# Kernel tuning notes

Hardware: AMD Instinct MI355X
Metric: run time of the kernel (lower is better)

Reference implementation:

```python
import jax, jax.numpy as jnp
import numpy as np

VOCAB = 32000
EMBED = 256
HID = 512
SOS_ID = 1
EOS_ID = 2
PAD_ID = 0


def setup_inputs() -> dict:
    key = jax.random.key(0)
    ks = jax.random.split(key, 8)
    B, L = 64, 49
    scale = 0.02
    return {
        "features": jax.random.normal(ks[0], (B, L, HID), jnp.float32),
        "emb": jax.random.normal(ks[1], (VOCAB, EMBED), jnp.float32) * scale,
        "W_ih": jax.random.normal(ks[2], (3 * HID, EMBED), jnp.float32) * scale,
        "W_hh": jax.random.normal(ks[3], (3 * HID, HID), jnp.float32) * scale,
        "b_ih": jax.random.normal(ks[4], (3 * HID,), jnp.float32) * scale,
        "b_hh": jax.random.normal(ks[5], (3 * HID,), jnp.float32) * scale,
        "W_out": jax.random.normal(ks[6], (VOCAB, HID), jnp.float32) * scale,
        "b_out": jax.random.normal(ks[7], (VOCAB,), jnp.float32) * scale,
        "max_len": 20,
    }


def _gru_cell(x, h, W_ih, W_hh, b_ih, b_hh):
    # torch.nn.GRUCell semantics (gates ordered r, z, n)
    gi = x @ W_ih.T + b_ih  # [B, 3H]
    gh = h @ W_hh.T + b_hh  # [B, 3H]
    i_r, i_z, i_n = jnp.split(gi, 3, axis=-1)
    h_r, h_z, h_n = jnp.split(gh, 3, axis=-1)
    r = jax.nn.sigmoid(i_r + h_r)
    z = jax.nn.sigmoid(i_z + h_z)
    n = jnp.tanh(i_n + r * h_n)
    return (1.0 - z) * n + z * h


def reference(features, emb, W_ih, W_hh, b_ih, b_hh, W_out, b_out, max_len):
    B = features.shape[0]
    h0 = features.mean(axis=1)  # [B, HID]
    x0 = emb[jnp.full((B,), SOS_ID, dtype=jnp.int32)]  # [B, EMBED]
    done0 = jnp.zeros((B,), dtype=bool)

    def step(carry, _):
        h, x, done = carry
        h = _gru_cell(x, h, W_ih, W_hh, b_ih, b_hh)
        logits = h @ W_out.T + b_out  # [B, VOCAB]
        pred = jnp.argmax(logits, axis=-1)  # [B]
        is_eos = pred == EOS_ID
        # original appends word only if sequence not complete and token != <EOS>
        tok = jnp.where(done | is_eos, PAD_ID, pred)
        done = done | is_eos
        x = emb[pred]  # greedy feedback
        return (h, x, done), (logits, tok)

    _, (logits, toks) = jax.lax.scan(step, (h0, x0, done0), None, length=max_len)
    # [T, B, V] -> [B, T, V]; [T, B] -> [B, T]
    return toks.T, jnp.transpose(logits, (1, 0, 2))
```

## Files before the change

### kernel.cpp

```cpp
#include <hip/hip_runtime.h>
#include <stdint.h>

#define VOCABN 32000
#define EMBEDN 256
#define HIDN   512
#define BN     64
#define SOSID  1
#define EOSID  2
#define NSUB   8

typedef __attribute__((ext_vector_type(8))) short short8;
typedef __attribute__((ext_vector_type(4))) float f32x4;

__device__ __forceinline__ unsigned ordf(float f) {
  unsigned u = __float_as_uint(f);
  return (u & 0x80000000u) ? ~u : (u | 0x80000000u);
}
__device__ __forceinline__ int decode_pred(unsigned long long pk) {
  return (int)(0xFFFFFFFFu - (unsigned)(pk & 0xFFFFFFFFull));
}
__device__ __forceinline__ unsigned short f2bf(float x) {
  unsigned u = __float_as_uint(x);
  unsigned r = (u + 0x7FFFu + ((u >> 16) & 1u)) >> 16;
  return (unsigned short)r;
}
__device__ __forceinline__ float bf2f(unsigned short h) {
  return __uint_as_float(((unsigned)h) << 16);
}
__device__ __forceinline__ f32x4 mfma3(short8 ah, short8 al, short8 bh, short8 bl,
                                       f32x4 acc) {
  acc = __builtin_amdgcn_mfma_f32_16x16x32_bf16(ah, bh, acc, 0, 0, 0);
  acc = __builtin_amdgcn_mfma_f32_16x16x32_bf16(ah, bl, acc, 0, 0, 0);
  acc = __builtin_amdgcn_mfma_f32_16x16x32_bf16(al, bh, acc, 0, 0, 0);
  return acc;
}

__global__ void k_init(const float* __restrict__ feat, float* __restrict__ h0,
                       int L, int* __restrict__ done, char* __restrict__ Hsp0) {
  int b = blockIdx.x, tid = threadIdx.x;
  float inv = 1.0f / (float)L;
  for (int j = tid; j < HIDN; j += 256) {
    const float* p = feat + (size_t)b * L * HIDN + j;
    float s = 0.f;
    for (int l = 0; l < L; ++l) s += p[(size_t)l * HIDN];
    float hv = s * inv;
    h0[b * HIDN + j] = hv;
    unsigned short hi = f2bf(hv);
    unsigned short lo = f2bf(hv - bf2f(hi));
    int bt = b >> 4, col = b & 15, kt = j >> 5, kr = j & 31;
    int ln = ((kr >> 3) << 4) | col, e = kr & 7;
    size_t off = (size_t)(bt * 16 + kt) * 2048 + ln * 16 + e * 2;
    *(unsigned short*)(Hsp0 + off) = hi;
    *(unsigned short*)(Hsp0 + off + 1024) = lo;
  }
  if (b == 0 && tid < 2 * BN) done[tid] = 0;
}

__global__ __launch_bounds__(256) void k_splitW(const float* __restrict__ W,
                                                char* __restrict__ Wsp,
                                                int ktshift, int K) {
  int tid = threadIdx.x, lane = tid & 63, tl = tid >> 6;
  int tile = blockIdx.x * 4 + tl;
  int vt = tile >> ktshift, kt = tile & ((1 << ktshift) - 1);
  int v = vt * 16 + (lane & 15);
  int k0 = kt * 32 + ((lane >> 4) << 3);
  const float* src = W + (size_t)v * K + k0;
  float xv[8];
  *(float4*)&xv[0] = *(const float4*)src;
  *(float4*)&xv[4] = *(const float4*)(src + 4);
  unsigned short h[8], l[8];
  #pragma unroll
  for (int i = 0; i < 8; ++i) {
    h[i] = f2bf(xv[i]);
    l[i] = f2bf(xv[i] - bf2f(h[i]));
  }
  uint4 H, Lw;
  H.x = (unsigned)h[0] | ((unsigned)h[1] << 16);
  H.y = (unsigned)h[2] | ((unsigned)h[3] << 16);
  H.z = (unsigned)h[4] | ((unsigned)h[5] << 16);
  H.w = (unsigned)h[6] | ((unsigned)h[7] << 16);
  Lw.x = (unsigned)l[0] | ((unsigned)l[1] << 16);
  Lw.y = (unsigned)l[2] | ((unsigned)l[3] << 16);
  Lw.z = (unsigned)l[4] | ((unsigned)l[5] << 16);
  Lw.w = (unsigned)l[6] | ((unsigned)l[7] << 16);
  char* dst = Wsp + (size_t)tile * 2048 + lane * 16;
  *(uint4*)dst = H;
  *(uint4*)(dst + 1024) = Lw;
}

__global__ __launch_bounds__(256) void k_gh(
    const float* __restrict__ emb, const char* __restrict__ Wihsp,
    const char* __restrict__ Whhsp, const float* __restrict__ b_ih,
    const float* __restrict__ b_hh, const float* __restrict__ h_rd,
    float* __restrict__ h_wr, const char* __restrict__ Hsp_rd,
    char* __restrict__ Hsp_wr,
    const unsigned long long* __restrict__ s_rd,
    unsigned long long* __restrict__ s_wr,
    const int* __restrict__ done_rd, int* __restrict__ done_wr,
    float* __restrict__ out_toks, int t, int T) {
  __shared__ int preds[16];
  __shared__ float red[3][4][256];
  int tid = threadIdx.x, lane = tid & 63, wid = tid >> 6;
  int jt = blockIdx.x >> 2, bt = blockIdx.x & 3;

  if (tid < 16) {
    int pr = SOSID;
    if (t) {
      unsigned long long mx = 0ull;
      #pragma unroll
      for (int s = 0; s < NSUB; ++s) {
        unsigned long long v = s_rd[s * BN + bt * 16 + tid];
        mx = (v > mx) ? v : mx;
      }
      pr = decode_pred(mx);
    }
    preds[tid] = pr;
  }
  if (blockIdx.x == 0) {
    s_wr[tid] = 0ull;
    s_wr[256 + tid] = 0ull;
    if (t >= 1 && tid < BN) {
      unsigned long long mx = 0ull;
      #pragma unroll
      for (int s = 0; s < NSUB; ++s) {
        unsigned long long v = s_rd[s * BN + tid];
        mx = (v > mx) ? v : mx;
      }
      int pred = decode_pred(mx);
      int iseos = (pred == EOSID) ? 1 : 0;
      int dold = done_rd[tid];
      out_toks[(size_t)tid * T + (t - 1)] = (float)((dold | iseos) ? 0 : pred);
      done_wr[tid] = dold | iseos;
    }
  }
  __syncthreads();

  int col = lane & 15, rg = lane >> 4;
  int xrow = preds[col];
  f32x4 acc_r = {0.f, 0.f, 0.f, 0.f}, acc_z = {0.f, 0.f, 0.f, 0.f};
  f32x4 acc_gin = {0.f, 0.f, 0.f, 0.f}, acc_ghn = {0.f, 0.f, 0.f, 0.f};

  #pragma unroll
  for (int u = 0; u < 6; ++u) {
    int g = wid * 6 + u;
    if (g < 8) {
      float xv[8];
      const float* src = emb + (size_t)xrow * EMBEDN + g * 32 + rg * 8;
      *(float4*)&xv[0] = *(const float4*)src;
      *(float4*)&xv[4] = *(const float4*)(src + 4);
      unsigned short hi[8], lo[8];
      #pragma unroll
      for (int i = 0; i < 8; ++i) {
        hi[i] = f2bf(xv[i]);
        lo[i] = f2bf(xv[i] - bf2f(hi[i]));
      }
      short8 xh, xl;
      #pragma unroll
      for (int i = 0; i < 8; ++i) { xh[i] = (short)hi[i]; xl[i] = (short)lo[i]; }
      const char* pr_ = Wihsp + (size_t)((jt) * 8 + g) * 2048 + lane * 16;
      const char* pz_ = Wihsp + (size_t)((32 + jt) * 8 + g) * 2048 + lane * 16;
      const char* pn_ = Wihsp + (size_t)((64 + jt) * 8 + g) * 2048 + lane * 16;
      acc_r = mfma3(*(const short8*)pr_, *(const short8*)(pr_ + 1024), xh, xl, acc_r);
      acc_z = mfma3(*(const short8*)pz_, *(const short8*)(pz_ + 1024), xh, xl, acc_z);
      acc_gin = mfma3(*(const short8*)pn_, *(const short8*)(pn_ + 1024), xh, xl, acc_gin);
    } else {
      int kt = g - 8;
      const char* bq = Hsp_rd + (size_t)(bt * 16 + kt) * 2048 + lane * 16;
      short8 hh = *(const short8*)bq;
      short8 hl = *(const short8*)(bq + 1024);
      const char* pr_ = Whhsp + (size_t)((jt) * 16 + kt) * 2048 + lane * 16;
      const char* pz_ = Whhsp + (size_t)((32 + jt) * 16 + kt) * 2048 + lane * 16;
      const char* pn_ = Whhsp + (size_t)((64 + jt) * 16 + kt) * 2048 + lane * 16;
      acc_r = mfma3(*(const short8*)pr_, *(const short8*)(pr_ + 1024), hh, hl, acc_r);
      acc_z = mfma3(*(const short8*)pz_, *(const short8*)(pz_ + 1024), hh, hl, acc_z);
      acc_ghn = mfma3(*(const short8*)pn_, *(const short8*)(pn_ + 1024), hh, hl, acc_ghn);
    }
  }

  if (wid) {
    *(f32x4*)&red[wid - 1][0][lane * 4] = acc_r;
    *(f32x4*)&red[wid - 1][1][lane * 4] = acc_z;
    *(f32x4*)&red[wid - 1][2][lane * 4] = acc_gin;
    *(f32x4*)&red[wid - 1][3][lane * 4] = acc_ghn;
  }
  __syncthreads();
  if (wid == 0) {
    #pragma unroll
    for (int w = 0; w < 3; ++w) {
      acc_r += *(f32x4*)&red[w][0][lane * 4];
      acc_z += *(f32x4*)&red[w][1][lane * 4];
      acc_gin += *(f32x4*)&red[w][2][lane * 4];
      acc_ghn += *(f32x4*)&red[w][3][lane * 4];
    }
    int j0 = jt * 16, j = j0 + rg * 4;
    int b = bt * 16 + col;
    float4 bir = *(const float4*)(b_ih + j);
    float4 bhr = *(const float4*)(b_hh + j);
    float4 biz = *(const float4*)(b_ih + 512 + j);
    float4 bhz = *(const float4*)(b_hh + 512 + j);
    float4 bin = *(const float4*)(b_ih + 1024 + j);
    float4 bhn = *(const float4*)(b_hh + 1024 + j);
    float bra[4] = {bir.x + bhr.x, bir.y + bhr.y, bir.z + bhr.z, bir.w + bhr.w};
    float bza[4] = {biz.x + bhz.x, biz.y + bhz.y, biz.z + bhz.z, biz.w + bhz.w};
    float bia[4] = {bin.x, bin.y, bin.z, bin.w};
    float bha[4] = {bhn.x, bhn.y, bhn.z, bhn.w};
    float4 hold = *(const float4*)(h_rd + (size_t)b * HIDN + j);
    float ho[4] = {hold.x, hold.y, hold.z, hold.w};
    float hn[4];
    unsigned short hi[4], lo[4];
    #pragma unroll
    for (int reg = 0; reg < 4; ++reg) {
      float r = 1.f / (1.f + expf(-(acc_r[reg] + bra[reg])));
      float z = 1.f / (1.f + expf(-(acc_z[reg] + bza[reg])));
      float n = tanhf(acc_gin[reg] + bia[reg] + r * (acc_ghn[reg] + bha[reg]));
      hn[reg] = (1.f - z) * n + z * ho[reg];
      hi[reg] = f2bf(hn[reg]);
      lo[reg] = f2bf(hn[reg] - bf2f(hi[reg]));
    }
    float4 hout = {hn[0], hn[1], hn[2], hn[3]};
    *(float4*)(h_wr + (size_t)b * HIDN + j) = hout;
    int kt2 = j >> 5, kr2 = j & 31;
    int ln2 = ((kr2 >> 3) << 4) | col, e2 = kr2 & 7;
    char* dst = Hsp_wr + ((size_t)((b >> 4) * 16 + kt2) * 2048 + ln2 * 16 + e2 * 2);
    uint2 Hp, Lp;
    Hp.x = (unsigned)hi[0] | ((unsigned)hi[1] << 16);
    Hp.y = (unsigned)hi[2] | ((unsigned)hi[3] << 16);
    Lp.x = (unsigned)lo[0] | ((unsigned)lo[1] << 16);
    Lp.y = (unsigned)lo[2] | ((unsigned)lo[3] << 16);
    *(uint2*)dst = Hp;
    *(uint2*)(dst + 1024) = Lp;
  }
}

__global__ __launch_bounds__(256) void k_logits6(
    const char* __restrict__ Wsp, const char* __restrict__ Hsp,
    const float* __restrict__ bout, float* __restrict__ out_logits,
    unsigned long long* __restrict__ slots, int t, int T) {
  __shared__ __align__(16) f32x4 red[4][4][2][64];
  int tid = threadIdx.x, lane = tid & 63, wid = tid >> 6;
  int v0 = blockIdx.x * 32, vt = v0 >> 4;
  int sub = blockIdx.x & (NSUB - 1);

  f32x4 acc[4][2];
  #pragma unroll
  for (int nb = 0; nb < 4; ++nb)
    #pragma unroll
    for (int mv = 0; mv < 2; ++mv)
      acc[nb][mv] = (f32x4){0.f, 0.f, 0.f, 0.f};

  #pragma unroll 2
  for (int kk = 0; kk < 4; ++kk) {
    int kt = wid * 4 + kk;
    short8 ah[4], al[4], wh[2], wl[2];
    #pragma unroll
    for (int nb = 0; nb < 4; ++nb) {
      const char* q = Hsp + (size_t)(nb * 16 + kt) * 2048 + lane * 16;
      ah[nb] = *(const short8*)q;
      al[nb] = *(const short8*)(q + 1024);
    }
    #pragma unroll
    for (int mv = 0; mv < 2; ++mv) {
      const char* p = Wsp + (size_t)((vt + mv) * 16 + kt) * 2048 + lane * 16;
      wh[mv] = *(const short8*)p;
      wl[mv] = *(const short8*)(p + 1024);
    }
    #pragma unroll
    for (int nb = 0; nb < 4; ++nb)
      #pragma unroll
      for (int mv = 0; mv < 2; ++mv)
        acc[nb][mv] = mfma3(ah[nb], al[nb], wh[mv], wl[mv], acc[nb][mv]);
  }

  #pragma unroll
  for (int nb = 0; nb < 4; ++nb)
    #pragma unroll
    for (int mv = 0; mv < 2; ++mv)
      red[wid][nb][mv][lane] = acc[nb][mv];
  __syncthreads();

  int nb = wid;
  f32x4 sum[2];
  #pragma unroll
  for (int mv = 0; mv < 2; ++mv)
    sum[mv] = red[0][nb][mv][lane] + red[1][nb][mv][lane] +
              red[2][nb][mv][lane] + red[3][nb][mv][lane];

  int col = lane & 15, rg = lane >> 4;
  float bvv[2] = {bout[v0 + col], bout[v0 + 16 + col]};
  unsigned long long key[4] = {0ull, 0ull, 0ull, 0ull};

  #pragma unroll
  for (int mv = 0; mv < 2; ++mv) {
    int v = v0 + mv * 16 + col;
    #pragma unroll
    for (int reg = 0; reg < 4; ++reg) {
      float val = sum[mv][reg] + bvv[mv];
      int b = nb * 16 + rg * 4 + reg;
      __builtin_nontemporal_store(
          val, out_logits + ((size_t)b * T + t) * VOCABN + v);
      unsigned long long pk = ((unsigned long long)ordf(val) << 32) |
                              (unsigned long long)(0xFFFFFFFFu - (unsigned)v);
      key[reg] = (pk > key[reg]) ? pk : key[reg];
    }
  }
  #pragma unroll
  for (int m = 1; m < 16; m <<= 1) {
    #pragma unroll
    for (int reg = 0; reg < 4; ++reg) {
      unsigned long long o = __shfl_xor(key[reg], m, 64);
      key[reg] = (o > key[reg]) ? o : key[reg];
    }
  }
  if (col == 0) {
    #pragma unroll
    for (int reg = 0; reg < 4; ++reg) {
      int b = nb * 16 + rg * 4 + reg;
      atomicMax(slots + sub * BN + b, key[reg]);
    }
  }
}

__global__ void k_final(const unsigned long long* __restrict__ slots,
                        const int* __restrict__ done_rd,
                        float* __restrict__ out_toks, int T) {
  int b = threadIdx.x;
  if (b < BN) {
    unsigned long long mx = 0ull;
    #pragma unroll
    for (int s = 0; s < NSUB; ++s) {
      unsigned long long v = slots[s * BN + b];
      mx = (v > mx) ? v : mx;
    }
    int pred = decode_pred(mx);
    int iseos = (pred == EOSID) ? 1 : 0;
    int tok = (done_rd[b] || iseos) ? 0 : pred;
    out_toks[(size_t)b * T + (T - 1)] = (float)tok;
  }
}

extern "C" void kernel_launch(void* const* d_in, const int* in_sizes, int n_in,
                              void* d_out, int out_size, void* d_ws, size_t ws_size,
                              hipStream_t stream) {
  const float* feat = (const float*)d_in[0];
  const float* emb  = (const float*)d_in[1];
  const float* W_ih = (const float*)d_in[2];
  const float* W_hh = (const float*)d_in[3];
  const float* b_ih = (const float*)d_in[4];
  const float* b_hh = (const float*)d_in[5];
  const float* Wout = (const float*)d_in[6];
  const float* bout = (const float*)d_in[7];

  int L = in_sizes[0] / (BN * HIDN);
  int T = out_size / (BN * (VOCABN + 1));
  if (T <= 0) T = 20;

  float* out_toks   = (float*)d_out;
  float* out_logits = (float*)d_out + (size_t)BN * T;

  char* w = (char*)d_ws;
  float* hbuf = (float*)w;  w += (size_t)2 * BN * HIDN * sizeof(float);
  int*   done = (int*)w;    w += (size_t)2 * BN * sizeof(int);
  w = (char*)(((uintptr_t)w + 511) & ~(uintptr_t)511);
  unsigned long long* slots2 = (unsigned long long*)w;
  w += (size_t)2 * NSUB * BN * sizeof(unsigned long long);
  w = (char*)(((uintptr_t)w + 511) & ~(uintptr_t)511);
  char* Hsp   = w;          w += (size_t)2 * 4 * 16 * 2048;
  char* Wihsp = w;          w += (size_t)96 * 8 * 2048;
  char* Whhsp = w;          w += (size_t)96 * 16 * 2048;
  char* Wsp   = w;          w += (size_t)2000 * 16 * 2048;

  k_init<<<BN, 256, 0, stream>>>(feat, hbuf, L, done, Hsp);
  k_splitW<<<2000 * 16 / 4, 256, 0, stream>>>(Wout, Wsp, 4, 512);
  k_splitW<<<96 * 8 / 4, 256, 0, stream>>>(W_ih, Wihsp, 3, 256);
  k_splitW<<<96 * 16 / 4, 256, 0, stream>>>(W_hh, Whhsp, 4, 512);

  for (int t = 0; t < T; ++t) {
    const float* h_rd = hbuf + (size_t)(t & 1) * BN * HIDN;
    float* h_wr       = hbuf + (size_t)((t + 1) & 1) * BN * HIDN;
    const char* Hsp_rd = Hsp + (size_t)(t & 1) * 131072;
    char* Hsp_wr       = Hsp + (size_t)((t + 1) & 1) * 131072;
    const unsigned long long* s_rd = slots2 + ((t + 1) & 1) * NSUB * BN;
    unsigned long long* s_wr       = slots2 + (t & 1) * NSUB * BN;
    const int* drd = done + (t & 1) * BN;
    int* dwr       = done + ((t + 1) & 1) * BN;

    k_gh<<<128, 256, 0, stream>>>(emb, Wihsp, Whhsp, b_ih, b_hh, h_rd, h_wr,
                                  Hsp_rd, Hsp_wr, s_rd, s_wr, drd, dwr,
                                  out_toks, t, T);
    k_logits6<<<VOCABN / 32, 256, 0, stream>>>(Wsp, Hsp_wr, bout, out_logits,
                                               s_wr, t, T);
  }
  k_final<<<1, 64, 0, stream>>>(slots2 + ((T - 1) & 1) * NSUB * BN,
                                done + (T & 1) * BN, out_toks, T);
}
```

Before: 591.7 us.

## Assign each wave its own vocab tile over full K, drop LDS reduction

Result: slower. 994.2 us (+68.0%).

```diff
diff --git a/kernel.cpp b/kernel.cpp
--- a/kernel.cpp
+++ b/kernel.cpp
@@ -232,91 +232,76 @@
   }
 }
 
-__global__ __launch_bounds__(256) void k_logits6(
+__global__ __launch_bounds__(256) void k_logits7(
     const char* __restrict__ Wsp, const char* __restrict__ Hsp,
     const float* __restrict__ bout, float* __restrict__ out_logits,
     unsigned long long* __restrict__ slots, int t, int T) {
-  __shared__ __align__(16) f32x4 red[4][4][2][64];
   int tid = threadIdx.x, lane = tid & 63, wid = tid >> 6;
-  int v0 = blockIdx.x * 32, vt = v0 >> 4;
+  int v0 = blockIdx.x * 64;
+  int vt = (v0 >> 4) + wid;
   int sub = blockIdx.x & (NSUB - 1);
 
-  f32x4 acc[4][2];
-  #pragma unroll
-  for (int nb = 0; nb < 4; ++nb)
-    #pragma unroll
-    for (int mv = 0; mv < 2; ++mv)
-      acc[nb][mv] = (f32x4){0.f, 0.f, 0.f, 0.f};
-
-  #pragma unroll 2
-  for (int kk = 0; kk < 4; ++kk) {
-    int kt = wid * 4 + kk;
-    short8 ah[4], al[4], wh[2], wl[2];
+  f32x4 acc[4];
+  #pragma unroll
+  for (int nb = 0; nb < 4; ++nb) acc[nb] = (f32x4){0.f, 0.f, 0.f, 0.f};
+
+  #pragma unroll 4
+  for (int kt = 0; kt < 16; ++kt) {
+    short8 ah[4], al[4];
     #pragma unroll
     for (int nb = 0; nb < 4; ++nb) {
       const char* q = Hsp + (size_t)(nb * 16 + kt) * 2048 + lane * 16;
       ah[nb] = *(const short8*)q;
       al[nb] = *(const short8*)(q + 1024);
     }
-    #pragma unroll
-    for (int mv = 0; mv < 2; ++mv) {
-      const char* p = Wsp + (size_t)((vt + mv) * 16 + kt) * 2048 + lane * 16;
-      wh[mv] = *(const short8*)p;
-      wl[mv] = *(const short8*)(p + 1024);
-    }
+    const char* p = Wsp + (size_t)(vt * 16 + kt) * 2048 + lane * 16;
+    short8 wh = __builtin_nontemporal_load((const short8*)p);
+    short8 wl = __builtin_nontemporal_load((const short8*)(p + 1024));
     #pragma unroll
     for (int nb = 0; nb < 4; ++nb)
-      #pragma unroll
-      for (int mv = 0; mv < 2; ++mv)
-        acc[nb][mv] = mfma3(ah[nb], al[nb], wh[mv], wl[mv], acc[nb][mv]);
-  }
-
+      acc[nb] = mfma3(ah[nb], al[nb], wh, wl, acc[nb]);
+  }
+
+  int col = lane & 15, rg = lane >> 4;
+  int v = vt * 16 + col;
+  float bv = bout[v];
+  unsigned long long key[4][4];
   #pragma unroll
   for (int nb = 0; nb < 4; ++nb)
     #pragma unroll
-    for (int mv = 0; mv < 2; ++mv)
-      red[wid][nb][mv][lane] = acc[nb][mv];
-  __syncthreads();
-
-  int nb = wid;
-  f32x4 sum[2];
-  #pragma unroll
-  for (int mv = 0; mv < 2; ++mv)
-    sum[mv] = red[0][nb][mv][lane] + red[1][nb][mv][lane] +
-              red[2][nb][mv][lane] + red[3][nb][mv][lane];
-
-  int col = lane & 15, rg = lane >> 4;
-  float bvv[2] = {bout[v0 + col], bout[v0 + 16 + col]};
-  unsigned long long key[4] = {0ull, 0ull, 0ull, 0ull};
-
-  #pragma unroll
-  for (int mv = 0; mv < 2; ++mv) {
-    int v = v0 + mv * 16 + col;
+    for (int reg = 0; reg < 4; ++reg) key[nb][reg] = 0ull;
+
+  #pragma unroll
+  for (int nb = 0; nb < 4; ++nb) {
     #pragma unroll
     for (int reg = 0; reg < 4; ++reg) {
-      float val = sum[mv][reg] + bvv[mv];
+      float val = acc[nb][reg] + bv;
       int b = nb * 16 + rg * 4 + reg;
       __builtin_nontemporal_store(
           val, out_logits + ((size_t)b * T + t) * VOCABN + v);
       unsigned long long pk = ((unsigned long long)ordf(val) << 32) |
                               (unsigned long long)(0xFFFFFFFFu - (unsigned)v);
-      key[reg] = (pk > key[reg]) ? pk : key[reg];
+      key[nb][reg] = (pk > key[nb][reg]) ? pk : key[nb][reg];
     }
   }
   #pragma unroll
   for (int m = 1; m < 16; m <<= 1) {
     #pragma unroll
-    for (int reg = 0; reg < 4; ++reg) {
-      unsigned long long o = __shfl_xor(key[reg], m, 64);
-      key[reg] = (o > key[reg]) ? o : key[reg];
-    }
+    for (int nb = 0; nb < 4; ++nb)
+      #pragma unroll
+      for (int reg = 0; reg < 4; ++reg) {
+        unsigned long long o = __shfl_xor(key[nb][reg], m, 64);
+        key[nb][reg] = (o > key[nb][reg]) ? o : key[nb][reg];
+      }
   }
   if (col == 0) {
     #pragma unroll
-    for (int reg = 0; reg < 4; ++reg) {
-      int b = nb * 16 + rg * 4 + reg;
-      atomicMax(slots + sub * BN + b, key[reg]);
-    }
+    for (int nb = 0; nb < 4; ++nb)
+      #pragma unroll
+      for (int reg = 0; reg < 4; ++reg) {
+        int b = nb * 16 + rg * 4 + reg;
+        atomicMax(slots + sub * BN + b, key[nb][reg]);
+      }
   }
 }
 
@@ -387,7 +372,7 @@
     k_gh<<<128, 256, 0, stream>>>(emb, Wihsp, Whhsp, b_ih, b_hh, h_rd, h_wr,
                                   Hsp_rd, Hsp_wr, s_rd, s_wr, drd, dwr,
                                   out_toks, t, T);
-    k_logits6<<<VOCABN / 32, 256, 0, stream>>>(Wsp, Hsp_wr, bout, out_logits,
+    k_logits7<<<VOCABN / 64, 256, 0, stream>>>(Wsp, Hsp_wr, bout, out_logits,
                                                s_wr, t, T);
   }
   k_final<<<1, 64, 0, stream>>>(slots2 + ((T - 1) & 1) * NSUB * BN,
```
